# Kernel optimization log

Hardware: AMD Instinct MI355X
Metric: run time of the kernel (lower is better)

The kernel has to match this reference:

```python
import jax, jax.numpy as jnp
import numpy as np

HID, KQ, V = 1024, 64, 64
B, S = 8, 2048
NEG_INF = -1000000000.0


def setup_inputs() -> dict:
    key = jax.random.key(0)
    ks = jax.random.split(key, 10)
    return {
        "k_hidden_inputs": jax.random.normal(ks[0], (B, S, HID), jnp.float32),
        "q_hidden_inputs": jax.random.normal(ks[1], (B, S, HID), jnp.float32),
        "v_hidden_inputs": jax.random.normal(ks[2], (B, S, HID), jnp.float32),
        "mask": jax.random.randint(ks[3], (B, S, S), 0, 2, jnp.int32),
        "Wq": jax.random.normal(ks[4], (HID, KQ), jnp.float32) * 0.02,
        "bq": jnp.zeros((KQ,), jnp.float32),
        "Wk": jax.random.normal(ks[5], (HID, KQ), jnp.float32) * 0.02,
        "bk": jnp.zeros((KQ,), jnp.float32),
        "Wv": jax.random.normal(ks[6], (HID, V), jnp.float32) * 0.02,
        "bv": jnp.zeros((V,), jnp.float32),
    }


def reference(k_hidden_inputs, q_hidden_inputs, v_hidden_inputs, mask,
              Wq, bq, Wk, bk, Wv, bv):
    keys = jnp.einsum('bsh,hd->bsd', k_hidden_inputs, Wk) + bk
    queries = jnp.einsum('bsh,hd->bsd', q_hidden_inputs, Wq) + bq
    values = jnp.einsum('bsh,hd->bsd', v_hidden_inputs, Wv) + bv
    # scaled dot-product scores: [B, S_q, S_k]
    scores = jnp.einsum('bqd,bkd->bqk', queries, keys) / jnp.sqrt(jnp.float32(KQ))
    scores = jnp.where(mask == 0, jnp.float32(NEG_INF), scores)
    attn = jax.nn.softmax(scores, axis=-1)
    return jnp.einsum('bqk,bkv->bqv', attn, values)
```

## Files before the change

### kernel.cpp

```cpp
#include <hip/hip_runtime.h>

#define HIDDEN 1024
#define NB 8
#define SEQ 2048
#define DH 64

typedef long long i64;
typedef unsigned short u16;
typedef __attribute__((ext_vector_type(8))) short short8;
typedef __attribute__((ext_vector_type(4))) float f32x4;

#define MFMA16 __builtin_amdgcn_mfma_f32_16x16x32_bf16

__device__ __forceinline__ u16 f2bf(float x) {
    unsigned u = __float_as_uint(x);
    u = u + 0x7FFFu + ((u >> 16) & 1u);
    return (u16)(u >> 16);
}
__device__ __forceinline__ float bf2f(u16 h) {
    return __uint_as_float(((unsigned)h) << 16);
}
__device__ __forceinline__ void gl_lds16(const void* g, void* l) {
    __builtin_amdgcn_global_load_lds(
        (const __attribute__((address_space(1))) unsigned int*)g,
        (__attribute__((address_space(3))) unsigned int*)l, 16, 0, 0);
}

__global__ __launch_bounds__(256) void wt_prep(
    const float* __restrict__ Wq, const float* __restrict__ Wk, const float* __restrict__ Wv,
    u16* __restrict__ Wth, u16* __restrict__ Wtl)
{
    const int te = blockIdx.x >> 4, hb = blockIdx.x & 15;
    const float* W = te == 0 ? Wq : te == 1 ? Wk : Wv;
    __shared__ float tile[64][65];
    const int t = threadIdx.x;
    const int hr = t >> 2, c0 = (t & 3) << 4;
    #pragma unroll
    for (int j = 0; j < 16; j += 4) {
        float4 w4 = *(const float4*)(W + (i64)(hb * 64 + hr) * DH + c0 + j);
        tile[hr][c0 + j] = w4.x; tile[hr][c0 + j + 1] = w4.y;
        tile[hr][c0 + j + 2] = w4.z; tile[hr][c0 + j + 3] = w4.w;
    }
    __syncthreads();
    const int n = t >> 2, h0 = (t & 3) << 4;
    const i64 base = (i64)te * DH * HIDDEN + (i64)n * HIDDEN + hb * 64 + h0;
    #pragma unroll
    for (int j = 0; j < 16; ++j) {
        float x = tile[h0 + j][n];
        u16 h = f2bf(x);
        Wth[base + j] = h;
        Wtl[base + j] = f2bf(x - bf2f(h));
    }
}

__global__ __launch_bounds__(256) void proj_mfma(
    const float* __restrict__ qh, const float* __restrict__ kh, const float* __restrict__ vh,
    const u16* __restrict__ Wth, const u16* __restrict__ Wtl,
    const float* __restrict__ bq, const float* __restrict__ bk, const float* __restrict__ bv,
    u16* __restrict__ Qb, u16* __restrict__ Kb, u16* __restrict__ Vt)
{
    const int te = blockIdx.y;
    const float* A    = te == 0 ? qh : te == 1 ? kh : vh;
    const float* bias = te == 0 ? bq : te == 1 ? bk : bv;
    const int row0 = blockIdx.x * 64;

    __shared__ __attribute__((aligned(16))) u16 Ah[64][72];
    __shared__ __attribute__((aligned(16))) u16 Al[64][72];
    __shared__ __attribute__((aligned(16))) u16 Bh[64][72];
    __shared__ __attribute__((aligned(16))) u16 Bl[64][72];

    const int t = threadIdx.x;
    const int lane = t & 63, w = t >> 6;
    const int lr = lane & 15, lg = lane >> 4;
    const int sr = t >> 2, sc = (t & 3) << 4;

    f32x4 acc[4] = {};
    const u16* WthT = Wth + (i64)te * DH * HIDDEN;
    const u16* WtlT = Wtl + (i64)te * DH * HIDDEN;

    for (int k0 = 0; k0 < HIDDEN; k0 += 64) {
        {
            short8 h0v, h1v, l0v, l1v;
            #pragma unroll
            for (int j = 0; j < 16; j += 4) {
                float4 a4 = *(const float4*)(A + (i64)(row0 + sr) * HIDDEN + k0 + sc + j);
                float xs[4] = {a4.x, a4.y, a4.z, a4.w};
                #pragma unroll
                for (int q = 0; q < 4; ++q) {
                    u16 h = f2bf(xs[q]);
                    u16 l = f2bf(xs[q] - bf2f(h));
                    if (j + q < 8) { h0v[j + q] = (short)h; l0v[j + q] = (short)l; }
                    else           { h1v[j + q - 8] = (short)h; l1v[j + q - 8] = (short)l; }
                }
            }
            *(short8*)&Ah[sr][sc]     = h0v;
            *(short8*)&Ah[sr][sc + 8] = h1v;
            *(short8*)&Al[sr][sc]     = l0v;
            *(short8*)&Al[sr][sc + 8] = l1v;
        }
        {
            const i64 gb = (i64)sr * HIDDEN + k0 + sc;
            *(short8*)&Bh[sr][sc]     = *(const short8*)(WthT + gb);
            *(short8*)&Bh[sr][sc + 8] = *(const short8*)(WthT + gb + 8);
            *(short8*)&Bl[sr][sc]     = *(const short8*)(WtlT + gb);
            *(short8*)&Bl[sr][sc + 8] = *(const short8*)(WtlT + gb + 8);
        }
        __syncthreads();

        short8 a_h[2], a_l[2];
        #pragma unroll
        for (int s = 0; s < 2; ++s) {
            a_h[s] = *(const short8*)&Ah[w * 16 + lr][s * 32 + lg * 8];
            a_l[s] = *(const short8*)&Al[w * 16 + lr][s * 32 + lg * 8];
        }
        #pragma unroll
        for (int nt = 0; nt < 4; ++nt) {
            #pragma unroll
            for (int s = 0; s < 2; ++s) {
                short8 b_h = *(const short8*)&Bh[nt * 16 + lr][s * 32 + lg * 8];
                short8 b_l = *(const short8*)&Bl[nt * 16 + lr][s * 32 + lg * 8];
                acc[nt] = MFMA16(a_h[s], b_h, acc[nt], 0, 0, 0);
                acc[nt] = MFMA16(a_h[s], b_l, acc[nt], 0, 0, 0);
                acc[nt] = MFMA16(a_l[s], b_h, acc[nt], 0, 0, 0);
            }
        }
        __syncthreads();
    }
    #pragma unroll
    for (int nt = 0; nt < 4; ++nt) {
        const int col = nt * 16 + lr;
        const float bb = bias[col];
        #pragma unroll
        for (int r = 0; r < 4; ++r) {
            const i64 grow = row0 + w * 16 + lg * 4 + r;
            const u16 v = f2bf(acc[nt][r] + bb);
            if (te == 0)      Qb[grow * DH + col] = v;
            else if (te == 1) Kb[grow * DH + col] = v;
            else {
                const i64 bb2 = grow >> 11, key = grow & 2047;
                Vt[(bb2 * DH + col) * SEQ + key] = v;
            }
        }
    }
}

__global__ __launch_bounds__(64) void attn_mfma(
    const u16* __restrict__ Qb, const u16* __restrict__ Kb, const u16* __restrict__ Vt,
    const int* __restrict__ mask, float* __restrict__ out)
{
    __shared__ __attribute__((aligned(16))) u16 Kl[2][64 * 64];
    __shared__ __attribute__((aligned(16))) u16 Vl[2][64 * 64];
    __shared__ __attribute__((aligned(16))) u16 Pl[16][72];

    const int lane = threadIdx.x;
    const int lr = lane & 15, lg = lane >> 4;
    const int b  = blockIdx.x >> 7;
    const int q0 = (blockIdx.x & 127) << 4;

    const i64 qrow = (i64)b * SEQ + q0 + lr;
    const short8 qf0 = *(const short8*)(Qb + qrow * DH + lg * 8);
    const short8 qf1 = *(const short8*)(Qb + qrow * DH + 32 + lg * 8);

    const int srow = lane >> 3;
    const int scb  = lane & 7;

    f32x4 oacc[4] = {};
    float rs0 = 0.f, rs1 = 0.f, rs2 = 0.f, rs3 = 0.f;

    {
        const i64 kbase = (i64)b * SEQ;
        #pragma unroll
        for (int i = 0; i < 8; ++i) {
            int row = i * 8 + srow, cb = scb ^ (row & 7);
            gl_lds16(Kb + (kbase + row) * DH + cb * 8, &Kl[0][i * 512]);
        }
        #pragma unroll
        for (int i = 0; i < 8; ++i) {
            int row = i * 8 + srow, cb = scb ^ (row & 7);
            gl_lds16(Vt + ((i64)b * DH + row) * SEQ + cb * 8, &Vl[0][i * 512]);
        }
    }

    #pragma unroll 1
    for (int t = 0; t < 32; ++t) {
        const int kt = t * 64;
        const int buf = t & 1;

        int mv[16];
        #pragma unroll
        for (int tt = 0; tt < 4; ++tt)
            #pragma unroll
            for (int r = 0; r < 4; ++r)
                mv[tt * 4 + r] =
                    mask[((i64)b * SEQ + q0 + lg * 4 + r) * SEQ + kt + tt * 16 + lr];

        if (t < 31) {
            const int kn = kt + 64;
            const i64 kbase = (i64)b * SEQ + kn;
            #pragma unroll
            for (int i = 0; i < 8; ++i) {
                int row = i * 8 + srow, cb = scb ^ (row & 7);
                gl_lds16(Kb + (kbase + row) * DH + cb * 8, &Kl[buf ^ 1][i * 512]);
            }
            #pragma unroll
            for (int i = 0; i < 8; ++i) {
                int row = i * 8 + srow, cb = scb ^ (row & 7);
                gl_lds16(Vt + ((i64)b * DH + row) * SEQ + kn + cb * 8, &Vl[buf ^ 1][i * 512]);
            }
            asm volatile("s_waitcnt vmcnt(32)" ::: "memory");
        } else {
            asm volatile("s_waitcnt vmcnt(16)" ::: "memory");
        }

        f32x4 sacc[4] = {};
        #pragma unroll
        for (int tt = 0; tt < 4; ++tt) {
            int row = tt * 16 + lr, x = row & 7;
            short8 k0 = *(const short8*)&Kl[buf][row * 64 + ((lg) ^ x) * 8];
            short8 k1 = *(const short8*)&Kl[buf][row * 64 + ((lg + 4) ^ x) * 8];
            sacc[tt] = MFMA16(qf0, k0, sacc[tt], 0, 0, 0);
            sacc[tt] = MFMA16(qf1, k1, sacc[tt], 0, 0, 0);
        }

        #pragma unroll
        for (int tt = 0; tt < 4; ++tt) {
            #pragma unroll
            for (int r = 0; r < 4; ++r) {
                float p = (mv[tt * 4 + r] != 0) ? __expf(sacc[tt][r] * 0.125f) : 0.0f;
                if      (r == 0) rs0 += p;
                else if (r == 1) rs1 += p;
                else if (r == 2) rs2 += p;
                else             rs3 += p;
                Pl[lg * 4 + r][tt * 16 + lr] = f2bf(p);
            }
        }

        const short8 p0 = *(const short8*)&Pl[lr][lg * 8];
        const short8 p1 = *(const short8*)&Pl[lr][32 + lg * 8];
        #pragma unroll
        for (int vt = 0; vt < 4; ++vt) {
            int row = vt * 16 + lr, x = row & 7;
            short8 v0 = *(const short8*)&Vl[buf][row * 64 + ((lg) ^ x) * 8];
            short8 v1 = *(const short8*)&Vl[buf][row * 64 + ((lg + 4) ^ x) * 8];
            oacc[vt] = MFMA16(p0, v0, oacc[vt], 0, 0, 0);
            oacc[vt] = MFMA16(p1, v1, oacc[vt], 0, 0, 0);
        }
    }

    float rs[4] = {rs0, rs1, rs2, rs3};
    #pragma unroll
    for (int r = 0; r < 4; ++r) {
        float v = rs[r];
        v += __shfl_xor(v, 1, 64);
        v += __shfl_xor(v, 2, 64);
        v += __shfl_xor(v, 4, 64);
        v += __shfl_xor(v, 8, 64);
        rs[r] = 1.0f / v;
    }
    #pragma unroll
    for (int vt = 0; vt < 4; ++vt)
        #pragma unroll
        for (int r = 0; r < 4; ++r)
            out[((i64)b * SEQ + q0 + lg * 4 + r) * DH + vt * 16 + lr] = oacc[vt][r] * rs[r];
}

extern "C" void kernel_launch(void* const* d_in, const int* in_sizes, int n_in,
                              void* d_out, int out_size, void* d_ws, size_t ws_size,
                              hipStream_t stream) {
    const float* kh   = (const float*)d_in[0];
    const float* qh   = (const float*)d_in[1];
    const float* vh   = (const float*)d_in[2];
    const int*   mask = (const int*)  d_in[3];
    const float* Wq   = (const float*)d_in[4];
    const float* bq   = (const float*)d_in[5];
    const float* Wk   = (const float*)d_in[6];
    const float* bk   = (const float*)d_in[7];
    const float* Wv   = (const float*)d_in[8];
    const float* bv   = (const float*)d_in[9];
    float* out = (float*)d_out;

    u16* Wth = (u16*)d_ws;
    u16* Wtl = Wth + 3 * DH * HIDDEN;
    u16* Qb  = Wtl + 3 * DH * HIDDEN;
    u16* Kb  = Qb + (i64)NB * SEQ * DH;
    u16* Vt  = Kb + (i64)NB * SEQ * DH;

    wt_prep<<<48, 256, 0, stream>>>(Wq, Wk, Wv, Wth, Wtl);
    proj_mfma<<<dim3(256, 3), 256, 0, stream>>>(qh, kh, vh, Wth, Wtl,
                                                bq, bk, bv, Qb, Kb, Vt);
    attn_mfma<<<1024, 64, 0, stream>>>(Qb, Kb, Vt, mask, out);
}
```

Before: 124.1 us.

## Rewrite projection as LDS-free single-wave MFMA with register-prefetched activations

Replaces the 256-thread LDS-tiled projection GEMM with a 64-thread single-wave kernel over 16-row tiles. Each lane loads its activation fragment straight from global memory into registers, with a one-step prefetch, and reads the weight hi/lo fragments directly from global, so no shared memory or barriers are needed. This removes LDS staging and syncthreads overhead and raises the block count to 3072. In exchange the weights are re-read from global (L2) by every wave instead of being shared through LDS, and the activation loads are less coalesced, strided by row per lane.

```diff
diff --git a/kernel.cpp b/kernel.cpp
--- a/kernel.cpp
+++ b/kernel.cpp
@@ -53,7 +53,7 @@
     }
 }
 
-__global__ __launch_bounds__(256) void proj_mfma(
+__global__ __launch_bounds__(64) void proj_mfma2(
     const float* __restrict__ qh, const float* __restrict__ kh, const float* __restrict__ vh,
     const u16* __restrict__ Wth, const u16* __restrict__ Wtl,
     const float* __restrict__ bq, const float* __restrict__ bk, const float* __restrict__ bv,
@@ -62,77 +62,55 @@
     const int te = blockIdx.y;
     const float* A    = te == 0 ? qh : te == 1 ? kh : vh;
     const float* bias = te == 0 ? bq : te == 1 ? bk : bv;
-    const int row0 = blockIdx.x * 64;
-
-    __shared__ __attribute__((aligned(16))) u16 Ah[64][72];
-    __shared__ __attribute__((aligned(16))) u16 Al[64][72];
-    __shared__ __attribute__((aligned(16))) u16 Bh[64][72];
-    __shared__ __attribute__((aligned(16))) u16 Bl[64][72];
-
-    const int t = threadIdx.x;
-    const int lane = t & 63, w = t >> 6;
+    const int row0 = blockIdx.x << 4;
+    const int lane = threadIdx.x;
     const int lr = lane & 15, lg = lane >> 4;
-    const int sr = t >> 2, sc = (t & 3) << 4;
+
+    const u16* WH = Wth + (i64)te * DH * HIDDEN;
+    const u16* WL = Wtl + (i64)te * DH * HIDDEN;
+    const float* arow = A + (i64)(row0 + lr) * HIDDEN + (lg << 3);
 
     f32x4 acc[4] = {};
-    const u16* WthT = Wth + (i64)te * DH * HIDDEN;
-    const u16* WtlT = Wtl + (i64)te * DH * HIDDEN;
-
-    for (int k0 = 0; k0 < HIDDEN; k0 += 64) {
+
+    float4 a0 = *(const float4*)(arow);
+    float4 a1 = *(const float4*)(arow + 4);
+
+    #pragma unroll 2
+    for (int k0 = 0; k0 < HIDDEN; k0 += 32) {
+        float4 n0 = a0, n1 = a1;
+        if (k0 + 32 < HIDDEN) {
+            n0 = *(const float4*)(arow + k0 + 32);
+            n1 = *(const float4*)(arow + k0 + 36);
+        }
+        short8 ah, al;
         {
-            short8 h0v, h1v, l0v, l1v;
-            #pragma unroll
-            for (int j = 0; j < 16; j += 4) {
-                float4 a4 = *(const float4*)(A + (i64)(row0 + sr) * HIDDEN + k0 + sc + j);
-                float xs[4] = {a4.x, a4.y, a4.z, a4.w};
-                #pragma unroll
-                for (int q = 0; q < 4; ++q) {
-                    u16 h = f2bf(xs[q]);
-                    u16 l = f2bf(xs[q] - bf2f(h));
-                    if (j + q < 8) { h0v[j + q] = (short)h; l0v[j + q] = (short)l; }
-                    else           { h1v[j + q - 8] = (short)h; l1v[j + q - 8] = (short)l; }
-                }
-            }
-            *(short8*)&Ah[sr][sc]     = h0v;
-            *(short8*)&Ah[sr][sc + 8] = h1v;
-            *(short8*)&Al[sr][sc]     = l0v;
-            *(short8*)&Al[sr][sc + 8] = l1v;
-        }
-        {
-            const i64 gb = (i64)sr * HIDDEN + k0 + sc;
-            *(short8*)&Bh[sr][sc]     = *(const short8*)(WthT + gb);
-            *(short8*)&Bh[sr][sc + 8] = *(const short8*)(WthT + gb + 8);
-            *(short8*)&Bl[sr][sc]     = *(const short8*)(WtlT + gb);
-            *(short8*)&Bl[sr][sc + 8] = *(const short8*)(WtlT + gb + 8);
-        }
-        __syncthreads();
-
-        short8 a_h[2], a_l[2];
-        #pragma unroll
-        for (int s = 0; s < 2; ++s) {
-            a_h[s] = *(const short8*)&Ah[w * 16 + lr][s * 32 + lg * 8];
-            a_l[s] = *(const short8*)&Al[w * 16 + lr][s * 32 + lg * 8];
+            const float xs[8] = {a0.x, a0.y, a0.z, a0.w, a1.x, a1.y, a1.z, a1.w};
+            #pragma unroll
+            for (int j = 0; j < 8; ++j) {
+                const u16 h = f2bf(xs[j]);
+                ah[j] = (short)h;
+                al[j] = (short)f2bf(xs[j] - bf2f(h));
+            }
         }
         #pragma unroll
         for (int nt = 0; nt < 4; ++nt) {
-            #pragma unroll
-            for (int s = 0; s < 2; ++s) {
-                short8 b_h = *(const short8*)&Bh[nt * 16 + lr][s * 32 + lg * 8];
-                short8 b_l = *(const short8*)&Bl[nt * 16 + lr][s * 32 + lg * 8];
-                acc[nt] = MFMA16(a_h[s], b_h, acc[nt], 0, 0, 0);
-                acc[nt] = MFMA16(a_h[s], b_l, acc[nt], 0, 0, 0);
-                acc[nt] = MFMA16(a_l[s], b_h, acc[nt], 0, 0, 0);
-            }
-        }
-        __syncthreads();
-    }
+            const i64 wb = (i64)(nt * 16 + lr) * HIDDEN + k0 + (lg << 3);
+            const short8 bh = *(const short8*)(WH + wb);
+            const short8 bl = *(const short8*)(WL + wb);
+            acc[nt] = MFMA16(ah, bh, acc[nt], 0, 0, 0);
+            acc[nt] = MFMA16(ah, bl, acc[nt], 0, 0, 0);
+            acc[nt] = MFMA16(al, bh, acc[nt], 0, 0, 0);
+        }
+        a0 = n0; a1 = n1;
+    }
+
     #pragma unroll
     for (int nt = 0; nt < 4; ++nt) {
         const int col = nt * 16 + lr;
         const float bb = bias[col];
         #pragma unroll
         for (int r = 0; r < 4; ++r) {
-            const i64 grow = row0 + w * 16 + lg * 4 + r;
+            const i64 grow = row0 + (lg << 2) + r;
             const u16 v = f2bf(acc[nt][r] + bb);
             if (te == 0)      Qb[grow * DH + col] = v;
             else if (te == 1) Kb[grow * DH + col] = v;
@@ -286,7 +264,7 @@
     u16* Vt  = Kb + (i64)NB * SEQ * DH;
 
     wt_prep<<<48, 256, 0, stream>>>(Wq, Wk, Wv, Wth, Wtl);
-    proj_mfma<<<dim3(256, 3), 256, 0, stream>>>(qh, kh, vh, Wth, Wtl,
-                                                bq, bk, bv, Qb, Kb, Vt);
+    proj_mfma2<<<dim3(1024, 3), 64, 0, stream>>>(qh, kh, vh, Wth, Wtl,
+                                                 bq, bk, bv, Qb, Kb, Vt);
     attn_mfma<<<1024, 64, 0, stream>>>(Qb, Kb, Vt, mask, out);
 }
```

New measurement: 193.1 us. 55.6% more time.
